# Optimization experiments

Hardware: AMD Instinct MI355X
Metric: run time of the kernel (lower is better)

## Reference

```python
import jax, jax.numpy as jnp
import numpy as np

N_NODES = 100000
N_EDGES = 1600000
IN_CH = 128
NHIDDEN = 64
OUT_CH = 40
NLAYERS = 4
ALPHA = 0.1


def setup_inputs() -> dict:
    key = jax.random.key(0)
    ks = jax.random.split(key, 7)
    x = jax.random.normal(ks[0], (N_NODES, IN_CH), dtype=jnp.float32)
    edge_index = jax.random.randint(ks[1], (2, N_EDGES), 0, N_NODES, dtype=jnp.int64)
    batch_graph = jnp.zeros((N_NODES,), dtype=jnp.int64)
    fc1_w = jax.random.normal(ks[2], (NHIDDEN, IN_CH), dtype=jnp.float32) * (1.0 / np.sqrt(IN_CH))
    fc1_b = jax.random.normal(ks[3], (NHIDDEN,), dtype=jnp.float32) * 0.01
    conv_w = jax.random.normal(ks[4], (NLAYERS, NHIDDEN, NHIDDEN), dtype=jnp.float32) * (1.0 / np.sqrt(NHIDDEN))
    fc2_w = jax.random.normal(ks[5], (OUT_CH, NHIDDEN), dtype=jnp.float32) * (1.0 / np.sqrt(NHIDDEN))
    fc2_b = jax.random.normal(ks[6], (OUT_CH,), dtype=jnp.float32) * 0.01
    return {"x": x, "edge_index": edge_index, "batch_graph": batch_graph,
            "fc1_w": fc1_w, "fc1_b": fc1_b, "conv_w": conv_w,
            "fc2_w": fc2_w, "fc2_b": fc2_b}


def reference(x, edge_index, batch_graph, fc1_w, fc1_b, conv_w, fc2_w, fc2_b):
    # eval mode: dropout layers are identity
    n = x.shape[0]
    row, col = edge_index[0], edge_index[1]  # source, target

    # gcn_norm with add_self_loops=False: sym deg^-1/2 normalization
    deg = jax.ops.segment_sum(jnp.ones_like(row, dtype=x.dtype), col, num_segments=n)
    dinv = jnp.where(deg > 0, deg ** -0.5, 0.0)
    norm = (dinv[row] * dinv[col])[:, None]  # [E, 1]

    h = jax.nn.relu(x @ fc1_w.T + fc1_b)  # [N, nhidden]
    h0 = h
    nlayers = conv_w.shape[0]
    for i in range(nlayers):
        # GCN2Conv: aggregate, initial-residual mix, weight1 matmul (beta=1)
        agg = jax.ops.segment_sum(h[row] * norm, col, num_segments=n)
        mixed = (1.0 - ALPHA) * agg + ALPHA * h0
        h = jax.nn.relu(mixed @ conv_w[i])
    out = h @ fc2_w.T + fc2_b  # [N, out_channels]
    return out
```

## Files before the change

kernel.cpp:

```cpp
#include <hip/hip_runtime.h>
#include <hip/hip_fp16.h>

#define N_NODES 100000
#define N_EDGES 1600000
#define IN_CH   128
#define NHID    64
#define OUT_CH  40
#define NBLK    391
#define NBUCK   196
#define BCAP    8960


__global__ __launch_bounds__(256) void k_scan1(const int* __restrict__ cnt,
                                               int* __restrict__ rowptr,
                                               int* __restrict__ bsum) {
    __shared__ int s[256];
    int t = threadIdx.x;
    int n = blockIdx.x * 256 + t;
    int v = (n < N_NODES) ? cnt[n] : 0;
    s[t] = v;
    __syncthreads();
    for (int off = 1; off < 256; off <<= 1) {
        int add = (t >= off) ? s[t - off] : 0;
        __syncthreads();
        s[t] += add;
        __syncthreads();
    }
    int incl = s[t];
    if (n < N_NODES) rowptr[n] = incl - v;
    if (t == 255) bsum[blockIdx.x] = incl;
}

__global__ __launch_bounds__(512) void k_scan2(int* __restrict__ bsum) {
    __shared__ int s[512];
    int t = threadIdx.x;
    int v = (t < NBLK) ? bsum[t] : 0;
    s[t] = v;
    __syncthreads();
    for (int off = 1; off < 512; off <<= 1) {
        int add = (t >= off) ? s[t - off] : 0;
        __syncthreads();
        s[t] += add;
        __syncthreads();
    }
    if (t < NBLK) bsum[t] = s[t] - v;
}

__global__ __launch_bounds__(256) void k_scan3(const int* __restrict__ cnt,
                                               const int* __restrict__ bsum,
                                               int* __restrict__ rowptr,
                                               float* __restrict__ dinv) {
    int n = blockIdx.x * 256 + threadIdx.x;
    if (n < N_NODES) {
        int rp = rowptr[n] + bsum[n >> 8];
        rowptr[n] = rp;
        int c = cnt[n];
        dinv[n] = (c > 0) ? rsqrtf((float)c) : 0.0f;
    }
    if (blockIdx.x == 0 && threadIdx.x == 0) rowptr[N_NODES] = N_EDGES;
}


__global__ __launch_bounds__(256) void k_scatA(const int* __restrict__ ei,
                                               int* __restrict__ bucketCnt,
                                               int2* __restrict__ ebufA) {
    __shared__ int hist[NBUCK];
    __shared__ int base[NBUCK];
    int t = threadIdx.x;
    int chunk = blockIdx.x * 4096;
    for (int i = t; i < NBUCK; i += 256) hist[i] = 0;
    __syncthreads();
#pragma unroll 4
    for (int i = 0; i < 16; i++) {
        int e = chunk + i * 256 + t;
        if (e < N_EDGES) atomicAdd(&hist[ei[N_EDGES + e] >> 9], 1);
    }
    __syncthreads();
    for (int b = t; b < NBUCK; b += 256) {
        int h = hist[b];
        base[b] = h ? atomicAdd(&bucketCnt[b], h) : 0;
    }
    __syncthreads();
#pragma unroll 4
    for (int i = 0; i < 16; i++) {
        int e = chunk + i * 256 + t;
        if (e < N_EDGES) {
            int r = ei[e], c = ei[N_EDGES + e];
            int pos = atomicAdd(&base[c >> 9], 1);
            ebufA[(size_t)(c >> 9) * BCAP + pos] = make_int2(r, c);
        }
    }
}


__global__ __launch_bounds__(256) void k_deg(const int2* __restrict__ ebufA,
                                             const int* __restrict__ bucketCnt,
                                             int* __restrict__ cnt) {
    __shared__ int hist[512];
    int b = blockIdx.x;
    int nodeB = b * 512;
    int t = threadIdx.x;
    for (int i = t; i < 512; i += 256) hist[i] = 0;
    __syncthreads();
    int nE = bucketCnt[b];
    const int2* src = ebufA + (size_t)b * BCAP;
    for (int i = t; i < nE; i += 256) atomicAdd(&hist[src[i].y - nodeB], 1);
    __syncthreads();
    for (int i = t; i < 512; i += 256) {
        int node = nodeB + i;
        if (node < N_NODES) cnt[node] = hist[i];
    }
}


__global__ __launch_bounds__(256) void k_scatB(const int2* __restrict__ ebufA,
                                               const int* __restrict__ bucketCnt,
                                               const float* __restrict__ dinv,
                                               const int* __restrict__ rowptr,
                                               int2* __restrict__ e8) {
    __shared__ int lcur[512];
    int b = blockIdx.x;
    int nodeB = b * 512;
    int t = threadIdx.x;
    for (int i = t; i < 512; i += 256) {
        int node = nodeB + i;
        lcur[i] = (node < N_NODES) ? rowptr[node] : 0;
    }
    __syncthreads();
    int nE = bucketCnt[b];
    const int2* src = ebufA + (size_t)b * BCAP;
    for (int i = t; i < nE; i += 256) {
        int2 rc = src[i];
        float w = dinv[rc.x] * dinv[rc.y];
        int pos = atomicAdd(&lcur[rc.y - nodeB], 1);
        e8[pos] = make_int2(rc.x, __float_as_int(w));
    }
}

__device__ __forceinline__ void store_h4(__half* dst, float a, float b, float c, float d) {
    union { uint2 u; __half2 h[2]; } pk;
    pk.h[0] = __floats2half2_rn(a, b);
    pk.h[1] = __floats2half2_rn(c, d);
    *(uint2*)dst = pk.u;
}


__global__ __launch_bounds__(256) void k_fc1(const float* __restrict__ x,
                                             const float* __restrict__ w,
                                             const float* __restrict__ b,
                                             float* __restrict__ h0,
                                             __half* __restrict__ h016) {
    __shared__ float wT[IN_CH * NHID];
    __shared__ float xs[64 * 132];
    int t = threadIdx.x;
    int nodeBase = blockIdx.x * 64;

    for (int id = t; id < IN_CH * NHID; id += 256) {
        int o = id >> 7, k = id & 127;
        wT[k * NHID + o] = w[id];
    }
    {
        int nl = t >> 2, seg = t & 3;
        int n = nodeBase + nl;
        float4* dst = (float4*)(xs + nl * 132 + seg * 32);
        if (n < N_NODES) {
            const float4* src = (const float4*)(x + (size_t)n * IN_CH + seg * 32);
#pragma unroll
            for (int q = 0; q < 8; q++) dst[q] = src[q];
        } else {
            float4 z = {0.f, 0.f, 0.f, 0.f};
#pragma unroll
            for (int q = 0; q < 8; q++) dst[q] = z;
        }
    }
    __syncthreads();

    int tx = t & 15, ty = t >> 4;
    int o0 = tx * 4, n0 = ty * 4;
    float c[4][4];
#pragma unroll
    for (int i = 0; i < 4; i++)
#pragma unroll
        for (int j = 0; j < 4; j++) c[i][j] = 0.f;

#pragma unroll 4
    for (int k = 0; k < IN_CH; k += 4) {
        float4 b0 = *(const float4*)&wT[(k + 0) * NHID + o0];
        float4 b1 = *(const float4*)&wT[(k + 1) * NHID + o0];
        float4 b2 = *(const float4*)&wT[(k + 2) * NHID + o0];
        float4 b3 = *(const float4*)&wT[(k + 3) * NHID + o0];
#pragma unroll
        for (int i = 0; i < 4; i++) {
            float4 a = *(const float4*)&xs[(n0 + i) * 132 + k];
            c[i][0] = fmaf(a.x, b0.x, fmaf(a.y, b1.x, fmaf(a.z, b2.x, fmaf(a.w, b3.x, c[i][0]))));
            c[i][1] = fmaf(a.x, b0.y, fmaf(a.y, b1.y, fmaf(a.z, b2.y, fmaf(a.w, b3.y, c[i][1]))));
            c[i][2] = fmaf(a.x, b0.z, fmaf(a.y, b1.z, fmaf(a.z, b2.z, fmaf(a.w, b3.z, c[i][2]))));
            c[i][3] = fmaf(a.x, b0.w, fmaf(a.y, b1.w, fmaf(a.z, b2.w, fmaf(a.w, b3.w, c[i][3]))));
        }
    }
    float4 bias = *(const float4*)&b[o0];
#pragma unroll
    for (int i = 0; i < 4; i++) {
        int n = nodeBase + n0 + i;
        if (n < N_NODES) {
            float4 v;
            v.x = fmaxf(c[i][0] + bias.x, 0.f);
            v.y = fmaxf(c[i][1] + bias.y, 0.f);
            v.z = fmaxf(c[i][2] + bias.z, 0.f);
            v.w = fmaxf(c[i][3] + bias.w, 0.f);
            *(float4*)&h0[(size_t)n * NHID + o0] = v;
            store_h4(&h016[(size_t)n * NHID + o0], v.x, v.y, v.z, v.w);
        }
    }
}


__global__ __launch_bounds__(256, 4) void k_conv(const __half* __restrict__ hin,
                                                 const float* __restrict__ h0,
                                                 const int* __restrict__ rowptr,
                                                 const int2* __restrict__ e8,
                                                 const float* __restrict__ W,
                                                 __half* __restrict__ hout) {
    __shared__ float mix[32 * 68];
    int t = threadIdx.x;
    int nodeBase = blockIdx.x * 32;
    int grp = t >> 3;
    int cg = (t & 7) * 8;

    int n = nodeBase + grp;
    int s = rowptr[n], e = rowptr[n + 1];
    int d = e - s;
    int hi = (d > 0) ? (e - 1) : 0;

    float acc[8];
#pragma unroll
    for (int i = 0; i < 8; i++) acc[i] = 0.f;

    int2  pm[4];
    float4 pv[4];
    if (d > 0) {
#pragma unroll
        for (int u = 0; u < 4; u++) pm[u] = e8[min(s + u, hi)];
#pragma unroll
        for (int u = 0; u < 4; u++) pv[u] = *(const float4*)&hin[(size_t)pm[u].x * NHID + cg];
    }

    for (int j = s; j < e; j += 4) {
        int2  cm[4];
        float4 cv[4];
#pragma unroll
        for (int u = 0; u < 4; u++) { cm[u] = pm[u]; cv[u] = pv[u]; }
        int jn = j + 4;
        if (jn < e) {
#pragma unroll
            for (int u = 0; u < 4; u++) pm[u] = e8[min(jn + u, hi)];
#pragma unroll
            for (int u = 0; u < 4; u++) pv[u] = *(const float4*)&hin[(size_t)pm[u].x * NHID + cg];
        }
#pragma unroll
        for (int u = 0; u < 4; u++) {
            float wgt = (j + u < e) ? __int_as_float(cm[u].y) : 0.f;
            const __half2* hp = (const __half2*)&cv[u];
#pragma unroll
            for (int q = 0; q < 4; q++) {
                float2 f = __half22float2(hp[q]);
                acc[q * 2 + 0] = fmaf(wgt, f.x, acc[q * 2 + 0]);
                acc[q * 2 + 1] = fmaf(wgt, f.y, acc[q * 2 + 1]);
            }
        }
    }

    {
        float4 h0a = *(const float4*)&h0[(size_t)n * NHID + cg];
        float4 h0b = *(const float4*)&h0[(size_t)n * NHID + cg + 4];
        float4 m0, m1;
        m0.x = fmaf(0.9f, acc[0], 0.1f * h0a.x);
        m0.y = fmaf(0.9f, acc[1], 0.1f * h0a.y);
        m0.z = fmaf(0.9f, acc[2], 0.1f * h0a.z);
        m0.w = fmaf(0.9f, acc[3], 0.1f * h0a.w);
        m1.x = fmaf(0.9f, acc[4], 0.1f * h0b.x);
        m1.y = fmaf(0.9f, acc[5], 0.1f * h0b.y);
        m1.z = fmaf(0.9f, acc[6], 0.1f * h0b.z);
        m1.w = fmaf(0.9f, acc[7], 0.1f * h0b.w);
        *(float4*)&mix[grp * 68 + cg] = m0;
        *(float4*)&mix[grp * 68 + cg + 4] = m1;
    }
    __syncthreads();

    int tx = t & 15, ty = t >> 4;
    int o0 = tx * 4, r0 = ty * 2;
    float c[2][4];
#pragma unroll
    for (int i = 0; i < 2; i++)
#pragma unroll
        for (int j = 0; j < 4; j++) c[i][j] = 0.f;

#pragma unroll 4
    for (int k = 0; k < NHID; k += 4) {
        float4 b0 = *(const float4*)&W[(k + 0) * NHID + o0];
        float4 b1 = *(const float4*)&W[(k + 1) * NHID + o0];
        float4 b2 = *(const float4*)&W[(k + 2) * NHID + o0];
        float4 b3 = *(const float4*)&W[(k + 3) * NHID + o0];
#pragma unroll
        for (int i = 0; i < 2; i++) {
            float4 a = *(const float4*)&mix[(r0 + i) * 68 + k];
            c[i][0] = fmaf(a.x, b0.x, fmaf(a.y, b1.x, fmaf(a.z, b2.x, fmaf(a.w, b3.x, c[i][0]))));
            c[i][1] = fmaf(a.x, b0.y, fmaf(a.y, b1.y, fmaf(a.z, b2.y, fmaf(a.w, b3.y, c[i][1]))));
            c[i][2] = fmaf(a.x, b0.z, fmaf(a.y, b1.z, fmaf(a.z, b2.z, fmaf(a.w, b3.z, c[i][2]))));
            c[i][3] = fmaf(a.x, b0.w, fmaf(a.y, b1.w, fmaf(a.z, b2.w, fmaf(a.w, b3.w, c[i][3]))));
        }
    }
#pragma unroll
    for (int i = 0; i < 2; i++) {
        int n2 = nodeBase + r0 + i;
        store_h4(&hout[(size_t)n2 * NHID + o0],
                 fmaxf(c[i][0], 0.f), fmaxf(c[i][1], 0.f),
                 fmaxf(c[i][2], 0.f), fmaxf(c[i][3], 0.f));
    }
}


__global__ __launch_bounds__(256) void k_fc2(const __half* __restrict__ h,
                                             const float* __restrict__ w,
                                             const float* __restrict__ b,
                                             float* __restrict__ out) {
    __shared__ float wT[NHID * 44];
    __shared__ float hs[64 * 68];
    int t = threadIdx.x;
    int nodeBase = blockIdx.x * 64;

    for (int id = t; id < NHID * OUT_CH; id += 256) {
        int o = id >> 6, k = id & 63;
        wT[k * 44 + o] = w[id];
    }
    {
        int nl = t >> 2, seg = t & 3;
        int n = nodeBase + nl;
        float* dst = hs + nl * 68 + seg * 16;
        if (n < N_NODES) {
            float4 raw0 = *(const float4*)&h[(size_t)n * NHID + seg * 16];
            float4 raw1 = *(const float4*)&h[(size_t)n * NHID + seg * 16 + 8];
            const __half2* hp0 = (const __half2*)&raw0;
            const __half2* hp1 = (const __half2*)&raw1;
#pragma unroll
            for (int q = 0; q < 4; q++) {
                float2 f = __half22float2(hp0[q]);
                dst[q * 2 + 0] = f.x;
                dst[q * 2 + 1] = f.y;
            }
#pragma unroll
            for (int q = 0; q < 4; q++) {
                float2 f = __half22float2(hp1[q]);
                dst[8 + q * 2 + 0] = f.x;
                dst[8 + q * 2 + 1] = f.y;
            }
        } else {
#pragma unroll
            for (int q = 0; q < 16; q++) dst[q] = 0.f;
        }
    }
    __syncthreads();

    if (t < 160) {
        int tx = t % 10, ty = t / 10;
        int o0 = tx * 4, n0 = ty * 4;
        float c[4][4];
#pragma unroll
        for (int i = 0; i < 4; i++)
#pragma unroll
            for (int j = 0; j < 4; j++) c[i][j] = 0.f;

#pragma unroll 4
        for (int k = 0; k < NHID; k += 4) {
            float4 b0 = *(const float4*)&wT[(k + 0) * 44 + o0];
            float4 b1 = *(const float4*)&wT[(k + 1) * 44 + o0];
            float4 b2 = *(const float4*)&wT[(k + 2) * 44 + o0];
            float4 b3 = *(const float4*)&wT[(k + 3) * 44 + o0];
#pragma unroll
            for (int i = 0; i < 4; i++) {
                float4 a = *(const float4*)&hs[(n0 + i) * 68 + k];
                c[i][0] = fmaf(a.x, b0.x, fmaf(a.y, b1.x, fmaf(a.z, b2.x, fmaf(a.w, b3.x, c[i][0]))));
                c[i][1] = fmaf(a.x, b0.y, fmaf(a.y, b1.y, fmaf(a.z, b2.y, fmaf(a.w, b3.y, c[i][1]))));
                c[i][2] = fmaf(a.x, b0.z, fmaf(a.y, b1.z, fmaf(a.z, b2.z, fmaf(a.w, b3.z, c[i][2]))));
                c[i][3] = fmaf(a.x, b0.w, fmaf(a.y, b1.w, fmaf(a.z, b2.w, fmaf(a.w, b3.w, c[i][3]))));
            }
        }
        float4 bias = *(const float4*)&b[o0];
#pragma unroll
        for (int i = 0; i < 4; i++) {
            int n = nodeBase + n0 + i;
            if (n < N_NODES) {
                float4 v;
                v.x = c[i][0] + bias.x;
                v.y = c[i][1] + bias.y;
                v.z = c[i][2] + bias.z;
                v.w = c[i][3] + bias.w;
                *(float4*)&out[(size_t)n * OUT_CH + o0] = v;
            }
        }
    }
}


extern "C" void kernel_launch(void* const* d_in, const int* in_sizes, int n_in,
                              void* d_out, int out_size, void* d_ws, size_t ws_size,
                              hipStream_t stream) {
    const float* x    = (const float*)d_in[0];
    const int*   ei   = (const int*)d_in[1];
    const float* fc1w = (const float*)d_in[3];
    const float* fc1b = (const float*)d_in[4];
    const float* cw   = (const float*)d_in[5];
    const float* fc2w = (const float*)d_in[6];
    const float* fc2b = (const float*)d_in[7];
    float* out = (float*)d_out;

    char* p = (char*)d_ws;
    auto alloc = [&](size_t bytes) { char* r = p; p += (bytes + 255) & ~(size_t)255; return r; };
    float*  h0     = (float*) alloc((size_t)N_NODES * NHID * 4);
    __half* h016   = (__half*)alloc((size_t)N_NODES * NHID * 2);
    __half* ha16   = (__half*)alloc((size_t)N_NODES * NHID * 2);
    __half* hb16   = (__half*)alloc((size_t)N_NODES * NHID * 2);
    int2*   e8     = (int2*)  alloc(((size_t)N_EDGES + 8) * 8);
    int2*   ebufA  = (int2*)  alloc((size_t)NBUCK * BCAP * 8);
    int*    cnt    = (int*)   alloc((size_t)N_NODES * 4);
    int*    rowptr = (int*)   alloc((size_t)(N_NODES + 1) * 4);
    int*    bCnt   = (int*)   alloc((size_t)NBUCK * 4);
    float*  dinv   = (float*) alloc((size_t)N_NODES * 4);
    int*    bsum   = (int*)   alloc(512 * 4);

    hipMemsetAsync(bCnt, 0, (size_t)NBUCK * 4, stream);
    k_scatA<<<(N_EDGES + 4095) / 4096, 256, 0, stream>>>(ei, bCnt, ebufA);
    k_deg  <<<NBUCK, 256, 0, stream>>>(ebufA, bCnt, cnt);
    k_scan1<<<NBLK, 256, 0, stream>>>(cnt, rowptr, bsum);
    k_scan2<<<1, 512, 0, stream>>>(bsum);
    k_scan3<<<NBLK, 256, 0, stream>>>(cnt, bsum, rowptr, dinv);
    k_scatB<<<NBUCK, 256, 0, stream>>>(ebufA, bCnt, dinv, rowptr, e8);

    int gb64 = (N_NODES + 63) / 64;
    int gb32 = N_NODES / 32;
    k_fc1 <<<gb64, 256, 0, stream>>>(x, fc1w, fc1b, h0, h016);
    k_conv<<<gb32, 256, 0, stream>>>(h016, h0, rowptr, e8, cw + 0 * NHID * NHID, ha16);
    k_conv<<<gb32, 256, 0, stream>>>(ha16, h0, rowptr, e8, cw + 1 * NHID * NHID, hb16);
    k_conv<<<gb32, 256, 0, stream>>>(hb16, h0, rowptr, e8, cw + 2 * NHID * NHID, ha16);
    k_conv<<<gb32, 256, 0, stream>>>(ha16, h0, rowptr, e8, cw + 3 * NHID * NHID, hb16);
    k_fc2 <<<gb64, 256, 0, stream>>>(hb16, fc2w, fc2b, out);
}
```

Measured before the change: 451.1 us.

## Read fc1 weights from global and swizzle x tile in LDS

The fc1 kernel no longer stages the transposed 32KB weight matrix in shared memory. Weights are now read directly from global memory and served from cache, since each thread's output column slice is uniform across a wavefront. The x tile drops its padding and uses an XOR swizzle to avoid bank conflicts. Thread roles are remapped so tx indexes nodes and ty indexes outputs, and occupancy is raised through launch bounds. This cuts LDS use and the per-block weight transpose, at the cost of more global and cache weight traffic.

```diff
diff --git a/kernel.cpp b/kernel.cpp
--- a/kernel.cpp
+++ b/kernel.cpp
@@ -145,38 +145,40 @@
 }
 
 
-__global__ __launch_bounds__(256) void k_fc1(const float* __restrict__ x,
-                                             const float* __restrict__ w,
-                                             const float* __restrict__ b,
-                                             float* __restrict__ h0,
-                                             __half* __restrict__ h016) {
-    __shared__ float wT[IN_CH * NHID];
-    __shared__ float xs[64 * 132];
+__global__ __launch_bounds__(256, 4) void k_fc1(const float* __restrict__ x,
+                                                const float* __restrict__ w,
+                                                const float* __restrict__ b,
+                                                float* __restrict__ h0,
+                                                __half* __restrict__ h016) {
+    __shared__ float xs[64 * 128];
     int t = threadIdx.x;
     int nodeBase = blockIdx.x * 64;
 
-    for (int id = t; id < IN_CH * NHID; id += 256) {
-        int o = id >> 7, k = id & 127;
-        wT[k * NHID + o] = w[id];
-    }
     {
         int nl = t >> 2, seg = t & 3;
         int n = nodeBase + nl;
-        float4* dst = (float4*)(xs + nl * 132 + seg * 32);
+        int swz = (nl >> 2) & 7;
+        float4* dstrow = (float4*)(xs + nl * 128);
         if (n < N_NODES) {
             const float4* src = (const float4*)(x + (size_t)n * IN_CH + seg * 32);
 #pragma unroll
-            for (int q = 0; q < 8; q++) dst[q] = src[q];
+            for (int q = 0; q < 8; q++) dstrow[(seg * 8 + q) ^ swz] = src[q];
         } else {
             float4 z = {0.f, 0.f, 0.f, 0.f};
 #pragma unroll
-            for (int q = 0; q < 8; q++) dst[q] = z;
+            for (int q = 0; q < 8; q++) dstrow[(seg * 8 + q) ^ swz] = z;
         }
     }
     __syncthreads();
 
     int tx = t & 15, ty = t >> 4;
-    int o0 = tx * 4, n0 = ty * 4;
+    int n0 = tx * 4, o0 = ty * 4;
+    int swz = tx & 7;
+    const float4* xrow0 = (const float4*)(xs + (n0 + 0) * 128);
+    const float4* xrow1 = (const float4*)(xs + (n0 + 1) * 128);
+    const float4* xrow2 = (const float4*)(xs + (n0 + 2) * 128);
+    const float4* xrow3 = (const float4*)(xs + (n0 + 3) * 128);
+
     float c[4][4];
 #pragma unroll
     for (int i = 0; i < 4; i++)
@@ -185,19 +187,25 @@
 
 #pragma unroll 4
     for (int k = 0; k < IN_CH; k += 4) {
-        float4 b0 = *(const float4*)&wT[(k + 0) * NHID + o0];
-        float4 b1 = *(const float4*)&wT[(k + 1) * NHID + o0];
-        float4 b2 = *(const float4*)&wT[(k + 2) * NHID + o0];
-        float4 b3 = *(const float4*)&wT[(k + 3) * NHID + o0];
+        int kg = (k >> 2) ^ swz;
+        float4 b0 = *(const float4*)&w[(size_t)(o0 + 0) * IN_CH + k];
+        float4 b1 = *(const float4*)&w[(size_t)(o0 + 1) * IN_CH + k];
+        float4 b2 = *(const float4*)&w[(size_t)(o0 + 2) * IN_CH + k];
+        float4 b3 = *(const float4*)&w[(size_t)(o0 + 3) * IN_CH + k];
+        float4 a0 = xrow0[kg];
+        float4 a1 = xrow1[kg];
+        float4 a2 = xrow2[kg];
+        float4 a3 = xrow3[kg];
 #pragma unroll
         for (int i = 0; i < 4; i++) {
-            float4 a = *(const float4*)&xs[(n0 + i) * 132 + k];
-            c[i][0] = fmaf(a.x, b0.x, fmaf(a.y, b1.x, fmaf(a.z, b2.x, fmaf(a.w, b3.x, c[i][0]))));
-            c[i][1] = fmaf(a.x, b0.y, fmaf(a.y, b1.y, fmaf(a.z, b2.y, fmaf(a.w, b3.y, c[i][1]))));
-            c[i][2] = fmaf(a.x, b0.z, fmaf(a.y, b1.z, fmaf(a.z, b2.z, fmaf(a.w, b3.z, c[i][2]))));
-            c[i][3] = fmaf(a.x, b0.w, fmaf(a.y, b1.w, fmaf(a.z, b2.w, fmaf(a.w, b3.w, c[i][3]))));
-        }
-    }
+            float4 a = (i == 0) ? a0 : (i == 1) ? a1 : (i == 2) ? a2 : a3;
+            c[i][0] = fmaf(a.x, b0.x, fmaf(a.y, b0.y, fmaf(a.z, b0.z, fmaf(a.w, b0.w, c[i][0]))));
+            c[i][1] = fmaf(a.x, b1.x, fmaf(a.y, b1.y, fmaf(a.z, b1.z, fmaf(a.w, b1.w, c[i][1]))));
+            c[i][2] = fmaf(a.x, b2.x, fmaf(a.y, b2.y, fmaf(a.z, b2.z, fmaf(a.w, b2.w, c[i][2]))));
+            c[i][3] = fmaf(a.x, b3.x, fmaf(a.y, b3.y, fmaf(a.z, b3.z, fmaf(a.w, b3.w, c[i][3]))));
+        }
+    }
+
     float4 bias = *(const float4*)&b[o0];
 #pragma unroll
     for (int i = 0; i < 4; i++) {
```

Result: faster. 440.2 us (-2.4%).
